# Kernel optimization log

Measured on AMD Instinct MI355X. Metric: run time of the kernel, lower is better.

## Reference

```python
import jax, jax.numpy as jnp
import numpy as np

SIZE = 84        # pupil size
SIZE_F = 167     # field grid size
X_PAD = 39       # pad for 90 -> 167
KNUM = 16        # number of phase kernels (== required batch size)
CENTER = 120     # center crop
NOISE = 0.003


def _disk_mask(M=SIZE, R=SIZE / 2.0):
    # get_amp: unit disk of radius R on an MxM grid
    x, y = np.meshgrid(np.arange(-(M - 1) / 2, M / 2), np.arange(-(M - 1) / 2, M / 2))
    return jnp.asarray((x ** 2 + y ** 2 <= R ** 2).astype(np.float32))


def setup_inputs() -> dict:
    key = jax.random.key(0)
    k1, k2, k3 = jax.random.split(key, 3)
    x = jax.random.uniform(k1, (16, 90, 90, 1), dtype=jnp.float32)
    P = jax.random.uniform(k2, (16, 84, 84), dtype=jnp.float32,
                           minval=-0.5 * np.pi, maxval=0.5 * np.pi)
    W3 = jax.random.normal(k3, (12800, 10), dtype=jnp.float32) * 0.01
    b3 = jnp.zeros((10,), dtype=jnp.float32)
    return {"x": x, "P": P, "W3": W3, "b3": b3}


def _forward(x, P, W3, b3):
    mask = _disk_mask()
    amp = jnp.sum(mask)  # normalization of the autocorrelation

    # --- input field: pad 90 -> 167, complex, fftshift/fft2/fftshift ---
    # NOTE: tf.signal.fftshift default shifts ALL axes (incl. batch); the two
    # shifts cancel on the batch axis, replicated faithfully here.
    xp = jnp.pad(x, ((0, 0), (X_PAD, X_PAD - 1), (X_PAD, X_PAD - 1), (0, 0)))[..., 0]
    xc = xp.astype(jnp.complex64)
    X = jnp.fft.fftshift(jnp.fft.fft2(jnp.fft.fftshift(xc)))  # [16,167,167]
    Xr = jnp.repeat(X, KNUM, axis=0)                          # [256,167,167]

    # --- OTF: FFT-accelerated autocorrelation of the pupil P_amp*exp(i*phase) ---
    Pc = (mask * jnp.cos(P) + 1j * mask * jnp.sin(P)).astype(jnp.complex64)  # [16,84,84]
    Pp = jnp.pad(Pc, ((0, 0), (42, 41), (42, 41)))                           # [16,167,167]
    F = jnp.fft.fft2(Pp)
    OTF = jnp.fft.fftshift(jnp.fft.ifft2(F * jnp.conj(F)))  # all-axes shift
    OTF = jnp.concatenate([OTF[8:], OTF[:8]], axis=0) / amp  # undoes batch roll

    # --- propagation: multiply in frequency domain, back to space ---
    y = Xr * jnp.tile(OTF, (KNUM, 1, 1))  # [256,167,167]
    y = jnp.fft.fftshift(jnp.fft.ifft2(jnp.fft.fftshift(y)))
    r = jnp.real(y).reshape(16, KNUM, SIZE_F, SIZE_F)
    # per image: kernels 0..7 minus kernels 8..15 -> channels
    d = jnp.transpose(r[:, :8] - r[:, 8:], (0, 2, 3, 1))  # [16,167,167,8]

    # additive noise (np.random in original; fixed key -> deterministic constant)
    d = d + NOISE * jax.random.normal(jax.random.key(42), d.shape, dtype=jnp.float32)

    # center crop, relu, 3x3/3 max-pool, flatten, softmax dense
    b = (SIZE_F + 1) // 2 - CENTER // 2  # 24
    c = jax.nn.relu(d[:, b:b + CENTER, b:b + CENTER, :])  # [16,120,120,8]
    pooled = jax.lax.reduce_window(c, -jnp.inf, jax.lax.max,
                                   (1, 3, 3, 1), (1, 3, 3, 1), 'VALID')  # [16,40,40,8]
    flat = pooled.reshape(16, -1)  # [16,12800]
    return jax.nn.softmax(flat @ W3 + b3)


def reference(x, P, W3, b3):
    return _forward(x, P, W3, b3)
```

## Files before the change

### kernel.cpp

```cpp
#include <hip/hip_runtime.h>
#include <math.h>

constexpr int N  = 167;
constexpr int NN = 167 * 167;
constexpr int NP = 90;
constexpr int MP = 84;
constexpr int CROP = 120;
constexpr int HCOL = 84;
constexpr int HALF_SZ = 1784896;

constexpr size_t SZ_MAT   = (size_t)NN * 2;
constexpr size_t OFF_M1   = 0;
constexpr size_t OFF_M1T  = OFF_M1 + SZ_MAT;
constexpr size_t OFF_WF   = OFF_M1T + SZ_MAT;
constexpr size_t OFF_M2   = OFF_WF + SZ_MAT;
constexpr size_t OFF_M2T  = OFF_M2 + SZ_MAT;
constexpr size_t OFF_M3   = OFF_M2T + SZ_MAT;
constexpr size_t OFF_M3T84= OFF_M3 + (size_t)CROP * N * 2;
constexpr size_t OFF_PHI2 = OFF_M3T84 + (size_t)HCOL * CROP * 2;
constexpr size_t OFF_AMP  = OFF_PHI2 + (size_t)N * 2;
constexpr size_t OFF_X    = OFF_AMP + 4;
constexpr size_t OFF_T1   = OFF_X  + (size_t)16 * N * HCOL * 2;
constexpr size_t OFF_A    = OFF_T1 + (size_t)16 * N * NP * 2;
constexpr size_t OFF_T2   = OFF_A  + (size_t)16 * NN * 2;
constexpr size_t OFF_BD   = OFF_T2 + (size_t)16 * N * MP * 2;
constexpr size_t OFF_T3   = OFF_BD + (size_t)8 * NN;
constexpr size_t OFF_OTF  = OFF_T3 + (size_t)8 * N * HCOL * 2;
constexpr size_t OFF_FLAT = OFF_OTF+ (size_t)8 * N * HCOL * 2;
constexpr size_t OFF_PC   = OFF_FLAT + (size_t)16 * 12800;
constexpr size_t WS_FLOATS = OFF_PC + (size_t)16 * MP * MP * 2;

__device__ __forceinline__ unsigned rotl32(unsigned x, int r) {
    return (x << r) | (x >> (32 - r));
}

__device__ float noise_at(unsigned idx) {
    unsigned c0, c1; int lane;
    if (idx < (unsigned)HALF_SZ) { c0 = idx; c1 = idx + HALF_SZ; lane = 0; }
    else                         { c0 = idx - HALF_SZ; c1 = idx; lane = 1; }
    const unsigned ks0 = 0u, ks1 = 42u, ks2 = 0x1BD11BDAu ^ 42u;
    unsigned x0 = c0 + ks0, x1 = c1 + ks1;
#define TFR(r) { x0 += x1; x1 = rotl32(x1, r); x1 ^= x0; }
    TFR(13) TFR(15) TFR(26) TFR(6)   x0 += ks1; x1 += ks2 + 1u;
    TFR(17) TFR(29) TFR(16) TFR(24)  x0 += ks2; x1 += ks0 + 2u;
    TFR(13) TFR(15) TFR(26) TFR(6)   x0 += ks0; x1 += ks1 + 3u;
    TFR(17) TFR(29) TFR(16) TFR(24)  x0 += ks1; x1 += ks2 + 4u;
    TFR(13) TFR(15) TFR(26) TFR(6)   x0 += ks2; x1 += ks0 + 5u;
#undef TFR
    unsigned bits = lane ? x1 : x0;
    float u01 = __uint_as_float((bits >> 9) | 0x3F800000u) - 1.0f;
    const float lo = -0.99999994f;
    float f = fmaxf(lo, u01 * 2.0f + lo);
    float w = -log1pf(-f * f);
    float p;
    if (w < 5.0f) {
        w -= 2.5f;
        p = 2.81022636e-08f;
        p = fmaf(p, w, 3.43273939e-07f);
        p = fmaf(p, w, -3.5233877e-06f);
        p = fmaf(p, w, -4.39150654e-06f);
        p = fmaf(p, w, 0.00021858087f);
        p = fmaf(p, w, -0.00125372503f);
        p = fmaf(p, w, -0.00417768164f);
        p = fmaf(p, w, 0.246640727f);
        p = fmaf(p, w, 1.50140941f);
    } else {
        w = sqrtf(w) - 3.0f;
        p = -0.000200214257f;
        p = fmaf(p, w, 0.000100950558f);
        p = fmaf(p, w, 0.00134934322f);
        p = fmaf(p, w, -0.00367342844f);
        p = fmaf(p, w, 0.00573950773f);
        p = fmaf(p, w, -0.0076224613f);
        p = fmaf(p, w, 0.00943887047f);
        p = fmaf(p, w, 1.00167406f);
        p = fmaf(p, w, 2.83297682f);
    }
    return 1.41421356237f * p * f;
}

__global__ void k_prep(const float* __restrict__ P, float* ws) {
    int bx = blockIdx.x, t = threadIdx.x;
    if (bx < 109) {
        __shared__ float2 wtab[N];
        const float TPI = (float)(6.283185307179586476925286766559 / 167.0);
        for (int i = t; i < N; i += 256) {
            float s, c; sincosf(TPI * (float)i, &s, &c);
            wtab[i] = make_float2(c, s);
        }
        __syncthreads();
        int id = bx * 256 + t;
        if (id >= NN) return;
        int k = id / N, m = id % N;
        const float inv = 1.0f / 167.0f;
        int t1 = ((k + 84) * ((m + 83) % N)) % N;
        float2 w1 = wtab[t1];
        ws[OFF_M1 + 2 * id] = w1.x;  ws[OFF_M1 + 2 * id + 1] = -w1.y;
        ws[OFF_M1T + 2 * (m * N + k)] = w1.x;  ws[OFF_M1T + 2 * (m * N + k) + 1] = -w1.y;
        int tw = (k * m) % N;
        float2 ww = wtab[tw];
        ws[OFF_WF + 2 * id] = ww.x;  ws[OFF_WF + 2 * id + 1] = -ww.y;
        int t2 = ((k + 84) * m) % N;
        float2 w2 = wtab[t2];
        ws[OFF_M2 + 2 * id] = w2.x * inv;  ws[OFF_M2 + 2 * id + 1] = w2.y * inv;
        ws[OFF_M2T + 2 * (m * N + k)] = w2.x * inv;  ws[OFF_M2T + 2 * (m * N + k) + 1] = w2.y * inv;
        if (k < CROP) {
            int t3 = ((k + 108) * ((m + 83) % N)) % N;
            float2 w3 = wtab[t3];
            ws[OFF_M3 + 2 * (k * N + m)] = w3.x * inv;  ws[OFF_M3 + 2 * (k * N + m) + 1] = w3.y * inv;
            if (m < HCOL) {
                ws[OFF_M3T84 + 2 * (m * CROP + k)] = w3.x * inv;
                ws[OFF_M3T84 + 2 * (m * CROP + k) + 1] = w3.y * inv;
            }
        }
        if (id < N) {
            float2 wp = wtab[(2 * id) % N];
            ws[OFF_PHI2 + 2 * id] = wp.x;
            ws[OFF_PHI2 + 2 * id + 1] = wp.y;
        }
    } else if (bx < 550) {
        int id = (bx - 109) * 256 + t;
        if (id >= 16 * MP * MP) return;
        int rc = id % (MP * MP);
        int r = rc / MP, c = rc % MP;
        float y = r - 41.5f, x = c - 41.5f;
        float2 v = {0.f, 0.f};
        if (x * x + y * y <= 1764.0f) {
            float sp, cp; sincosf(P[id], &sp, &cp);
            v.x = cp; v.y = sp;
        }
        ((float2*)(ws + OFF_PC))[id] = v;
    } else {
        __shared__ int red[256];
        int cnt = 0;
        for (int i = t; i < MP * MP; i += 256) {
            int r = i / MP, c = i % MP;
            float y = r - 41.5f, x = c - 41.5f;
            if (x * x + y * y <= 1764.0f) cnt++;
        }
        red[t] = cnt; __syncthreads();
        for (int s = 128; s > 0; s >>= 1) { if (t < s) red[t] += red[t + s]; __syncthreads(); }
        if (t == 0) ws[OFF_AMP] = (float)red[0];
    }
}

__global__ __launch_bounds__(128) void k_rows(const float* __restrict__ x, float* ws) {
    int kr = blockIdx.x, bj = blockIdx.y, t = threadIdx.x;
    __shared__ float2 wbuf[NP];
    if (blockIdx.z == 0) {
        const float2* M1 = (const float2*)(ws + OFF_M1);
        if (t < NP) wbuf[t] = M1[kr * N + 39 + t];
        __syncthreads();
        if (t >= NP) return;
        float2 acc = {0.f, 0.f};
        for (int nr = 0; nr < NP; nr++) {
            float2 w = wbuf[nr];
            float xv = x[(bj * NP + nr) * NP + t];
            acc.x += w.x * xv; acc.y += w.y * xv;
        }
        ((float2*)(ws + OFF_T1))[(bj * N + kr) * NP + t] = acc;
    } else {
        const float2* WF = (const float2*)(ws + OFF_WF);
        if (t < MP) wbuf[t] = WF[kr * N + 42 + t];
        __syncthreads();
        if (t >= MP) return;
        const float2* PC = (const float2*)(ws + OFF_PC) + (size_t)bj * MP * MP;
        float2 acc = {0.f, 0.f};
        for (int nr = 0; nr < MP; nr++) {
            float2 w = wbuf[nr];
            float2 pc = PC[nr * MP + t];
            acc.x += w.x * pc.x - w.y * pc.y;
            acc.y += w.x * pc.y + w.y * pc.x;
        }
        ((float2*)(ws + OFF_T2))[(bj * N + kr) * MP + t] = acc;
    }
}

constexpr int RCH = 6;
__global__ __launch_bounds__(192) void k_cols(float* ws) {
    int bj = blockIdx.y, tid = threadIdx.x;
    __shared__ __align__(16) float2 sbuf[RCH * MP];
    if (blockIdx.x < 84) {
        int k0 = blockIdx.x * 2;
        const float2* T1 = (const float2*)(ws + OFF_T1);
        for (int idx = tid; idx < 2 * NP; idx += 192) {
            int r = idx / NP, m = idx % NP;
            if (k0 + r < N) sbuf[r * NP + m] = T1[((size_t)bj * N + k0 + r) * NP + m];
        }
        __syncthreads();
        int col = tid % HCOL, grp = tid / HCOL;
        if (grp >= 2) return;
        int kr = k0 + grp;
        if (kr >= N) return;
        const float2* M1T = (const float2*)(ws + OFF_M1T);
        float2 acc = {0.f, 0.f};
#pragma unroll 5
        for (int ncp = 0; ncp < 45; ncp++) {
            int nc = 2 * ncp;
            float4 u = *(const float4*)&sbuf[grp * NP + nc];
            float2 w0 = M1T[(39 + nc) * N + col];
            float2 w1 = M1T[(40 + nc) * N + col];
            acc.x += u.x * w0.x - u.y * w0.y;
            acc.y += u.x * w0.y + u.y * w0.x;
            acc.x += u.z * w1.x - u.w * w1.y;
            acc.y += u.z * w1.y + u.w * w1.x;
        }
        ((float2*)(ws + OFF_X))[((size_t)bj * N + kr) * HCOL + col] = acc;
    } else {
        int i0 = (blockIdx.x - 84) * RCH;
        const float2* T2 = (const float2*)(ws + OFF_T2);
        for (int idx = tid; idx < RCH * MP; idx += 192) {
            int q = idx / MP, nc = idx % MP, kr = i0 + q;
            if (kr < N) sbuf[idx] = T2[(bj * N + kr) * MP + nc];
        }
        __syncthreads();
        if (tid >= N) return;
        const float2* WF = (const float2*)(ws + OFF_WF);
        float2 acc[RCH];
#pragma unroll
        for (int q = 0; q < RCH; q++) acc[q] = make_float2(0.f, 0.f);
        for (int ncp = 0; ncp < 42; ncp++) {
            int nc = 2 * ncp;
            float2 w0 = WF[(42 + nc) * N + tid];
            float2 w1 = WF[(43 + nc) * N + tid];
#pragma unroll
            for (int q = 0; q < RCH; q++) {
                float4 u = *(const float4*)&sbuf[q * MP + nc];
                acc[q].x += u.x * w0.x - u.y * w0.y;
                acc[q].y += u.x * w0.y + u.y * w0.x;
                acc[q].x += u.z * w1.x - u.w * w1.y;
                acc[q].y += u.z * w1.y + u.w * w1.x;
            }
        }
        float2* A = (float2*)(ws + OFF_A);
#pragma unroll
        for (int q = 0; q < RCH; q++)
            if (i0 + q < N) A[((size_t)bj * N + i0 + q) * N + tid] = acc[q];
    }
}

__global__ __launch_bounds__(192) void k2c(float* ws) {
    int chunk = blockIdx.x, c = blockIdx.y, tid = threadIdx.x;
    int k0 = chunk * 2;
    __shared__ float bds[2][N];
    const float2* A = (const float2*)(ws + OFF_A);
    float inv_amp = 1.0f / ws[OFF_AMP];
    for (int idx = tid; idx < 2 * N; idx += 192) {
        int r = idx / N, m = idx % N;
        int k = k0 + r;
        if (k < N) {
            float2 a0 = A[((size_t)c * N + k) * N + m];
            float2 a1 = A[((size_t)(c + 8) * N + k) * N + m];
            bds[r][m] = (a0.x * a0.x + a0.y * a0.y - a1.x * a1.x - a1.y * a1.y) * inv_amp;
        }
    }
    __syncthreads();
    int col = tid % HCOL, grp = tid / HCOL;
    if (grp >= 2) return;
    int k = k0 + grp;
    if (k >= N) return;
    const float2* M2T = (const float2*)(ws + OFF_M2T);
    float2 acc = {0.f, 0.f};
    for (int m = 0; m < N; m++) {
        float bv = bds[grp][m];
        float2 w = M2T[m * N + col];
        acc.x += w.x * bv; acc.y += w.y * bv;
    }
    ((float2*)(ws + OFF_T3))[((size_t)c * N + k) * HCOL + col] = acc;
}

__global__ __launch_bounds__(192) void k2d(float* ws) {
    int chunk = blockIdx.x, c = blockIdx.y, tid = threadIdx.x;
    int i0 = chunk * 2;
    __shared__ float2 m2s[2][N];
    const float2* M2 = (const float2*)(ws + OFF_M2);
    for (int idx = tid; idx < 2 * N; idx += 192) {
        int r = idx / N, k = idx % N;
        if (i0 + r < N) m2s[r][k] = M2[(i0 + r) * N + k];
    }
    __syncthreads();
    int col = tid % HCOL, grp = tid / HCOL;
    if (grp >= 2) return;
    int i = i0 + grp;
    if (i >= N) return;
    const float2* T3 = (const float2*)(ws + OFF_T3) + (size_t)c * N * HCOL;
    float2 acc = {0.f, 0.f};
    for (int k = 0; k < N; k++) {
        float2 w = m2s[grp][k];
        float2 u = T3[k * HCOL + col];
        acc.x += u.x * w.x - u.y * w.y;
        acc.y += u.x * w.y + u.y * w.x;
    }
    ((float2*)(ws + OFF_OTF))[((size_t)c * N + i) * HCOL + col] = acc;
}

constexpr int K34R = 12;
constexpr int KCH  = 12;
constexpr int NT34 = (N + KCH - 1) / KCH;

constexpr int SM_ZS   = 0;
constexpr int SM_M3C  = SM_ZS + 2 * KCH * HCOL * 2;
constexpr int SM_PHIS = SM_M3C + 2 * KCH * K34R * 2;
constexpr int SM_PM   = SM_PHIS + N * 2;
constexpr int SM_TOT  = SM_PM + 4 * CROP;

constexpr int ZBUF = KCH * HCOL;
constexpr int MBUF = KCH * K34R;

#define K34_FMA_BODY(kl)                                                        \
    {                                                                           \
        float4 zz = *(const float4*)&zcur[(kl) * HCOL + 2 * pair];              \
        float4 wa = *(const float4*)&mcur[(kl) * K34R + r0];                    \
        a00.x += wa.x * zz.x - wa.y * zz.y;  a00.y += wa.x * zz.y + wa.y * zz.x;\
        a01.x += wa.x * zz.z - wa.y * zz.w;  a01.y += wa.x * zz.w + wa.y * zz.z;\
        a10.x += wa.z * zz.x - wa.w * zz.y;  a10.y += wa.z * zz.y + wa.w * zz.x;\
        a11.x += wa.z * zz.z - wa.w * zz.w;  a11.y += wa.z * zz.w + wa.w * zz.z;\
    }

__global__ __launch_bounds__(256) void k34(float* ws) {
    int chunk = blockIdx.x, c = blockIdx.y, b = blockIdx.z, tid = threadIdx.x;
    int i0 = chunk * K34R;
    __shared__ __align__(16) float smem[SM_TOT];
    float2* zbase = (float2*)(smem + SM_ZS);
    float2* mbase = (float2*)(smem + SM_M3C);
    float2* phis  = (float2*)(smem + SM_PHIS);
    float*  pmf   = smem + SM_PM;
    float2 (*us)[HCOL] = (float2 (*)[HCOL])(smem + SM_ZS);

    const float2* M3 = (const float2*)(ws + OFF_M3);
    const float4* X4   = (const float4*)(ws + OFF_X   + (size_t)b * N * HCOL * 2);
    const float4* OTF4 = (const float4*)(ws + OFF_OTF + (size_t)c * N * HCOL * 2);
    for (int idx = tid; idx < N; idx += 256) phis[idx] = ((const float2*)(ws + OFF_PHI2))[idx];

    int qkl[2], qcp[2];
#pragma unroll
    for (int e = 0; e < 2; e++) {
        int idx = tid + e * 256;
        qkl[e] = idx / 42; qcp[e] = idx - qkl[e] * 42;
    }
    int mkl = tid % 12, mr = tid / 12;

    int pair = tid % 42, grp = tid / 42;
    int r0 = grp * 2;
    float2 a00 = {0.f,0.f}, a01 = {0.f,0.f}, a10 = {0.f,0.f}, a11 = {0.f,0.f};

    float4 xq[2], oq[2];
    float2 m3r;

#pragma unroll
    for (int e = 0; e < 2; e++)
        if (qkl[e] < KCH) { xq[e] = X4[qkl[e] * 42 + qcp[e]]; oq[e] = OTF4[qkl[e] * 42 + qcp[e]]; }
    if (tid < 144) m3r = M3[(i0 + mr) * N + mkl];
#pragma unroll
    for (int e = 0; e < 2; e++)
        if (qkl[e] < KCH) {
            float4 z;
            z.x = xq[e].x * oq[e].x - xq[e].y * oq[e].y;
            z.y = xq[e].x * oq[e].y + xq[e].y * oq[e].x;
            z.z = xq[e].z * oq[e].z - xq[e].w * oq[e].w;
            z.w = xq[e].z * oq[e].w + xq[e].w * oq[e].z;
            *(float4*)&zbase[qkl[e] * HCOL + 2 * qcp[e]] = z;
        }
    if (tid < 144) mbase[mkl * K34R + mr] = m3r;
    __syncthreads();

    for (int t = 0; t < NT34; t++) {
        int cbuf = t & 1, nbuf = cbuf ^ 1;
        int kr0 = t * KCH;
        int chn = min(KCH, N - kr0);
        int nbase = kr0 + KCH;
        int nchn = (t + 1 < NT34) ? (N - nbase < KCH ? N - nbase : KCH) : 0;
        if (nchn > 0) {
#pragma unroll
            for (int e = 0; e < 2; e++)
                if (qkl[e] < nchn) { xq[e] = X4[(nbase + qkl[e]) * 42 + qcp[e]];
                                     oq[e] = OTF4[(nbase + qkl[e]) * 42 + qcp[e]]; }
            if (tid < 144 && mkl < nchn) m3r = M3[(i0 + mr) * N + nbase + mkl];
        }
        const float2* zcur = zbase + cbuf * ZBUF;
        const float2* mcur = mbase + cbuf * MBUF;
        if (grp < 6) {
            if (chn == KCH) {
#pragma unroll
                for (int kl = 0; kl < KCH; kl++) K34_FMA_BODY(kl)
            } else {
#pragma unroll
                for (int kl = 0; kl < KCH - 1; kl++) K34_FMA_BODY(kl)
            }
        }
        if (nchn > 0) {
            float2* znxt = zbase + nbuf * ZBUF;
            float2* mnxt = mbase + nbuf * MBUF;
#pragma unroll
            for (int e = 0; e < 2; e++)
                if (qkl[e] < nchn) {
                    float4 z;
                    z.x = xq[e].x * oq[e].x - xq[e].y * oq[e].y;
                    z.y = xq[e].x * oq[e].y + xq[e].y * oq[e].x;
                    z.z = xq[e].z * oq[e].z - xq[e].w * oq[e].w;
                    z.w = xq[e].z * oq[e].w + xq[e].w * oq[e].z;
                    *(float4*)&znxt[qkl[e] * HCOL + 2 * qcp[e]] = z;
                }
            if (tid < 144 && mkl < nchn) mnxt[mkl * K34R + mr] = m3r;
        }
        __syncthreads();
    }

    if (grp < 6) {
        *(float4*)&us[r0][2 * pair]     = make_float4(a00.x, a00.y, a01.x, a01.y);
        *(float4*)&us[r0 + 1][2 * pair] = make_float4(a10.x, a10.y, a11.x, a11.y);
    }
    __syncthreads();

    if (tid < 240) {
        int grp2 = tid / CROP, j = tid % CROP;
        int rbase = grp2 * 6;
        const float2* M3T84 = (const float2*)(ws + OFF_M3T84);
        float2 A[6]; float Bq[6];
#pragma unroll
        for (int q = 0; q < 6; q++) A[q] = make_float2(0.f, 0.f);
#pragma unroll 4
        for (int ncp = 0; ncp < 41; ncp++) {
            int nc = 2 * ncp;
            float2 w0 = M3T84[nc * CROP + j];
            float2 w1 = M3T84[(nc + 1) * CROP + j];
#pragma unroll
            for (int q = 0; q < 6; q++) {
                float4 u = *(const float4*)&us[rbase + q][nc];
                A[q].x += u.x * w0.x - u.y * w0.y;
                A[q].y += u.x * w0.y + u.y * w0.x;
                A[q].x += u.z * w1.x - u.w * w1.y;
                A[q].y += u.z * w1.y + u.w * w1.x;
            }
        }
        {
            float2 w = M3T84[82 * CROP + j];
#pragma unroll
            for (int q = 0; q < 6; q++) {
                float2 u = us[rbase + q][82];
                A[q].x += u.x * w.x - u.y * w.y;
                A[q].y += u.x * w.y + u.y * w.x;
            }
        }
        {
            float2 w = M3T84[(HCOL - 1) * CROP + j];
#pragma unroll
            for (int q = 0; q < 6; q++) {
                float2 u = us[rbase + q][HCOL - 1];
                Bq[q] = u.x * w.x - u.y * w.y;
            }
        }
#pragma unroll
        for (int g = 0; g < 2; g++) {
            float vmax = 0.f;
#pragma unroll
            for (int r = 0; r < 3; r++) {
                int q = g * 3 + r, i = i0 + rbase + q;
                int s = i + j + 49; if (s >= N) s -= N;
                float2 ph = phis[s];
                float val = A[q].x * (1.0f + ph.x) - A[q].y * ph.y + Bq[q];
                unsigned idx = (((unsigned)b * N + (24 + i)) * N + (24 + j)) * 8u + c;
                val += 0.003f * noise_at(idx);
                vmax = fmaxf(vmax, val);
            }
            pmf[(grp2 * 2 + g) * CROP + j] = vmax;
        }
    }
    __syncthreads();
    if (tid < 160) {
        int pr = tid / 40, pc = tid % 40;
        float m = fmaxf(fmaxf(pmf[pr * CROP + 3 * pc], pmf[pr * CROP + 3 * pc + 1]),
                        pmf[pr * CROP + 3 * pc + 2]);
        int prow = chunk * 4 + pr;
        ws[OFF_FLAT + (size_t)b * 12800 + ((size_t)prow * 40 + pc) * 8 + c] = m;
    }
}

__global__ void k5(const float* __restrict__ W3, const float* __restrict__ b3,
                   const float* __restrict__ ws, float* __restrict__ out) {
    int b = blockIdx.x, t = threadIdx.x;
    __shared__ float red[256][10];
    float acc[10];
#pragma unroll
    for (int o = 0; o < 10; o++) acc[o] = 0.f;
    const float* fl = ws + OFF_FLAT + (size_t)b * 12800;
    for (int f = t; f < 12800; f += 256) {
        float v = fl[f];
#pragma unroll
        for (int o = 0; o < 10; o++) acc[o] = fmaf(v, W3[f * 10 + o], acc[o]);
    }
#pragma unroll
    for (int o = 0; o < 10; o++) red[t][o] = acc[o];
    __syncthreads();
    for (int s = 128; s > 0; s >>= 1) {
        if (t < s) {
#pragma unroll
            for (int o = 0; o < 10; o++) red[t][o] += red[t + s][o];
        }
        __syncthreads();
    }
    if (t == 0) {
        float lg[10], mx = -1e30f;
#pragma unroll
        for (int o = 0; o < 10; o++) { lg[o] = red[0][o] + b3[o]; mx = fmaxf(mx, lg[o]); }
        float sum = 0.f;
#pragma unroll
        for (int o = 0; o < 10; o++) { lg[o] = expf(lg[o] - mx); sum += lg[o]; }
#pragma unroll
        for (int o = 0; o < 10; o++) out[b * 10 + o] = lg[o] / sum;
    }
}

extern "C" void kernel_launch(void* const* d_in, const int* in_sizes, int n_in,
                              void* d_out, int out_size, void* d_ws, size_t ws_size,
                              hipStream_t stream) {
    const float* x  = (const float*)d_in[0];
    const float* P  = (const float*)d_in[1];
    const float* W3 = (const float*)d_in[2];
    const float* b3 = (const float*)d_in[3];
    float* ws  = (float*)d_ws;
    float* out = (float*)d_out;

    k_prep<<<551, 256, 0, stream>>>(P, ws);
    k_rows<<<dim3(N, 16, 2), 128, 0, stream>>>(x, ws);
    k_cols<<<dim3(84 + 28, 16), 192, 0, stream>>>(ws);
    k2c<<<dim3(84, 8), 192, 0, stream>>>(ws);
    k2d<<<dim3(84, 8), 192, 0, stream>>>(ws);
    k34<<<dim3(CROP / K34R, 8, 16), 256, 0, stream>>>(ws);
    k5<<<16, 256, 0, stream>>>(W3, b3, ws, out);
}
```

Baseline: 205.7 us.

## Fuse row/column DFT stages and OTF squaring into fewer kernels

Merges the separate row and column DFT passes for the input field into one kernel that keeps the intermediate in shared memory. It also fuses the pupil DFT, the squared-magnitude difference and the first inverse OTF pass into a single kernel, which drops the A buffer round trip and two launches. Twiddle-table prep now writes the transposed matrices with coalesced indexing in separate blocks, and M2 is read from M2T. The cost is less parallelism per launch, and the pupil rows are recomputed per block pair.

```diff
diff --git a/kernel.cpp b/kernel.cpp
--- a/kernel.cpp
+++ b/kernel.cpp
@@ -81,7 +81,7 @@
 
 __global__ void k_prep(const float* __restrict__ P, float* ws) {
     int bx = blockIdx.x, t = threadIdx.x;
-    if (bx < 109) {
+    if (bx < 258) {
         __shared__ float2 wtab[N];
         const float TPI = (float)(6.283185307179586476925286766559 / 167.0);
         for (int i = t; i < N; i += 256) {
@@ -89,37 +89,49 @@
             wtab[i] = make_float2(c, s);
         }
         __syncthreads();
-        int id = bx * 256 + t;
-        if (id >= NN) return;
-        int k = id / N, m = id % N;
         const float inv = 1.0f / 167.0f;
-        int t1 = ((k + 84) * ((m + 83) % N)) % N;
-        float2 w1 = wtab[t1];
-        ws[OFF_M1 + 2 * id] = w1.x;  ws[OFF_M1 + 2 * id + 1] = -w1.y;
-        ws[OFF_M1T + 2 * (m * N + k)] = w1.x;  ws[OFF_M1T + 2 * (m * N + k) + 1] = -w1.y;
-        int tw = (k * m) % N;
-        float2 ww = wtab[tw];
-        ws[OFF_WF + 2 * id] = ww.x;  ws[OFF_WF + 2 * id + 1] = -ww.y;
-        int t2 = ((k + 84) * m) % N;
-        float2 w2 = wtab[t2];
-        ws[OFF_M2 + 2 * id] = w2.x * inv;  ws[OFF_M2 + 2 * id + 1] = w2.y * inv;
-        ws[OFF_M2T + 2 * (m * N + k)] = w2.x * inv;  ws[OFF_M2T + 2 * (m * N + k) + 1] = w2.y * inv;
-        if (k < CROP) {
-            int t3 = ((k + 108) * ((m + 83) % N)) % N;
+        if (bx < 109) {
+            int id = bx * 256 + t;
+            if (id >= NN) return;
+            int k = id / N, m = id % N;
+            int t1 = ((k + 84) * ((m + 83) % N)) % N;
+            float2 w1 = wtab[t1];
+            ws[OFF_M1 + 2 * id] = w1.x;  ws[OFF_M1 + 2 * id + 1] = -w1.y;
+            int tw = (k * m) % N;
+            float2 ww = wtab[tw];
+            ws[OFF_WF + 2 * id] = ww.x;  ws[OFF_WF + 2 * id + 1] = -ww.y;
+            if (k < CROP) {
+                int t3 = ((k + 108) * ((m + 83) % N)) % N;
+                float2 w3 = wtab[t3];
+                ws[OFF_M3 + 2 * (k * N + m)] = w3.x * inv;
+                ws[OFF_M3 + 2 * (k * N + m) + 1] = w3.y * inv;
+            }
+            if (id < N) {
+                float2 wp = wtab[(2 * id) % N];
+                ws[OFF_PHI2 + 2 * id] = wp.x;
+                ws[OFF_PHI2 + 2 * id + 1] = wp.y;
+            }
+        } else if (bx < 218) {
+            int id = (bx - 109) * 256 + t;
+            if (id >= NN) return;
+            int m = id / N, k = id % N;
+            int t1 = ((k + 84) * ((m + 83) % N)) % N;
+            float2 w1 = wtab[t1];
+            ws[OFF_M1T + 2 * id] = w1.x;  ws[OFF_M1T + 2 * id + 1] = -w1.y;
+            int t2 = ((k + 84) * m) % N;
+            float2 w2 = wtab[t2];
+            ws[OFF_M2T + 2 * id] = w2.x * inv;  ws[OFF_M2T + 2 * id + 1] = w2.y * inv;
+        } else {
+            int id = (bx - 218) * 256 + t;
+            if (id >= HCOL * CROP) return;
+            int m = id / CROP, kk = id % CROP;
+            int t3 = ((kk + 108) * ((m + 83) % N)) % N;
             float2 w3 = wtab[t3];
-            ws[OFF_M3 + 2 * (k * N + m)] = w3.x * inv;  ws[OFF_M3 + 2 * (k * N + m) + 1] = w3.y * inv;
-            if (m < HCOL) {
-                ws[OFF_M3T84 + 2 * (m * CROP + k)] = w3.x * inv;
-                ws[OFF_M3T84 + 2 * (m * CROP + k) + 1] = w3.y * inv;
-            }
-        }
-        if (id < N) {
-            float2 wp = wtab[(2 * id) % N];
-            ws[OFF_PHI2 + 2 * id] = wp.x;
-            ws[OFF_PHI2 + 2 * id + 1] = wp.y;
-        }
-    } else if (bx < 550) {
-        int id = (bx - 109) * 256 + t;
+            ws[OFF_M3T84 + 2 * id] = w3.x * inv;
+            ws[OFF_M3T84 + 2 * id + 1] = w3.y * inv;
+        }
+    } else if (bx < 699) {
+        int id = (bx - 258) * 256 + t;
         if (id >= 16 * MP * MP) return;
         int rc = id % (MP * MP);
         int r = rc / MP, c = rc % MP;
@@ -144,139 +156,128 @@
     }
 }
 
-__global__ __launch_bounds__(128) void k_rows(const float* __restrict__ x, float* ws) {
-    int kr = blockIdx.x, bj = blockIdx.y, t = threadIdx.x;
-    __shared__ float2 wbuf[NP];
-    if (blockIdx.z == 0) {
-        const float2* M1 = (const float2*)(ws + OFF_M1);
-        if (t < NP) wbuf[t] = M1[kr * N + 39 + t];
-        __syncthreads();
-        if (t >= NP) return;
-        float2 acc = {0.f, 0.f};
-        for (int nr = 0; nr < NP; nr++) {
-            float2 w = wbuf[nr];
-            float xv = x[(bj * NP + nr) * NP + t];
-            acc.x += w.x * xv; acc.y += w.y * xv;
-        }
-        ((float2*)(ws + OFF_T1))[(bj * N + kr) * NP + t] = acc;
-    } else {
-        const float2* WF = (const float2*)(ws + OFF_WF);
-        if (t < MP) wbuf[t] = WF[kr * N + 42 + t];
-        __syncthreads();
-        if (t >= MP) return;
-        const float2* PC = (const float2*)(ws + OFF_PC) + (size_t)bj * MP * MP;
-        float2 acc = {0.f, 0.f};
-        for (int nr = 0; nr < MP; nr++) {
-            float2 w = wbuf[nr];
-            float2 pc = PC[nr * MP + t];
-            acc.x += w.x * pc.x - w.y * pc.y;
-            acc.y += w.x * pc.y + w.y * pc.x;
-        }
-        ((float2*)(ws + OFF_T2))[(bj * N + kr) * MP + t] = acc;
-    }
-}
-
-constexpr int RCH = 6;
-__global__ __launch_bounds__(192) void k_cols(float* ws) {
-    int bj = blockIdx.y, tid = threadIdx.x;
-    __shared__ __align__(16) float2 sbuf[RCH * MP];
-    if (blockIdx.x < 84) {
-        int k0 = blockIdx.x * 2;
-        const float2* T1 = (const float2*)(ws + OFF_T1);
-        for (int idx = tid; idx < 2 * NP; idx += 192) {
-            int r = idx / NP, m = idx % NP;
-            if (k0 + r < N) sbuf[r * NP + m] = T1[((size_t)bj * N + k0 + r) * NP + m];
-        }
-        __syncthreads();
-        int col = tid % HCOL, grp = tid / HCOL;
-        if (grp >= 2) return;
-        int kr = k0 + grp;
-        if (kr >= N) return;
-        const float2* M1T = (const float2*)(ws + OFF_M1T);
-        float2 acc = {0.f, 0.f};
-#pragma unroll 5
-        for (int ncp = 0; ncp < 45; ncp++) {
-            int nc = 2 * ncp;
-            float4 u = *(const float4*)&sbuf[grp * NP + nc];
-            float2 w0 = M1T[(39 + nc) * N + col];
-            float2 w1 = M1T[(40 + nc) * N + col];
-            acc.x += u.x * w0.x - u.y * w0.y;
-            acc.y += u.x * w0.y + u.y * w0.x;
-            acc.x += u.z * w1.x - u.w * w1.y;
-            acc.y += u.z * w1.y + u.w * w1.x;
-        }
-        ((float2*)(ws + OFF_X))[((size_t)bj * N + kr) * HCOL + col] = acc;
-    } else {
-        int i0 = (blockIdx.x - 84) * RCH;
-        const float2* T2 = (const float2*)(ws + OFF_T2);
-        for (int idx = tid; idx < RCH * MP; idx += 192) {
-            int q = idx / MP, nc = idx % MP, kr = i0 + q;
-            if (kr < N) sbuf[idx] = T2[(bj * N + kr) * MP + nc];
-        }
-        __syncthreads();
-        if (tid >= N) return;
-        const float2* WF = (const float2*)(ws + OFF_WF);
-        float2 acc[RCH];
-#pragma unroll
-        for (int q = 0; q < RCH; q++) acc[q] = make_float2(0.f, 0.f);
-        for (int ncp = 0; ncp < 42; ncp++) {
-            int nc = 2 * ncp;
-            float2 w0 = WF[(42 + nc) * N + tid];
-            float2 w1 = WF[(43 + nc) * N + tid];
-#pragma unroll
-            for (int q = 0; q < RCH; q++) {
-                float4 u = *(const float4*)&sbuf[q * MP + nc];
-                acc[q].x += u.x * w0.x - u.y * w0.y;
-                acc[q].y += u.x * w0.y + u.y * w0.x;
-                acc[q].x += u.z * w1.x - u.w * w1.y;
-                acc[q].y += u.z * w1.y + u.w * w1.x;
-            }
-        }
-        float2* A = (float2*)(ws + OFF_A);
-#pragma unroll
-        for (int q = 0; q < RCH; q++)
-            if (i0 + q < N) A[((size_t)bj * N + i0 + q) * N + tid] = acc[q];
-    }
-}
-
-__global__ __launch_bounds__(192) void k2c(float* ws) {
-    int chunk = blockIdx.x, c = blockIdx.y, tid = threadIdx.x;
-    int k0 = chunk * 2;
-    __shared__ float bds[2][N];
-    const float2* A = (const float2*)(ws + OFF_A);
-    float inv_amp = 1.0f / ws[OFF_AMP];
-    for (int idx = tid; idx < 2 * N; idx += 192) {
-        int r = idx / N, m = idx % N;
-        int k = k0 + r;
-        if (k < N) {
-            float2 a0 = A[((size_t)c * N + k) * N + m];
-            float2 a1 = A[((size_t)(c + 8) * N + k) * N + m];
-            bds[r][m] = (a0.x * a0.x + a0.y * a0.y - a1.x * a1.x - a1.y * a1.y) * inv_amp;
+__global__ __launch_bounds__(192) void k_rcx(const float* __restrict__ x, float* ws) {
+    int kp = blockIdx.x, bj = blockIdx.y, tid = threadIdx.x;
+    int k0 = kp * 2;
+    __shared__ float2 m1w[2][NP];
+    __shared__ __align__(16) float2 t1s[2][NP];
+    const float2* M1 = (const float2*)(ws + OFF_M1);
+    for (int idx = tid; idx < 2 * NP; idx += 192) {
+        int r = idx / NP, m = idx % NP;
+        if (k0 + r < N) m1w[r][m] = M1[(k0 + r) * N + 39 + m];
+    }
+    __syncthreads();
+    {
+        int grp = tid / 96, tcol = tid % 96;
+        if (tcol < NP && k0 + grp < N) {
+            float2 acc = {0.f, 0.f};
+            for (int nr = 0; nr < NP; nr++) {
+                float2 w = m1w[grp][nr];
+                float xv = x[(bj * NP + nr) * NP + tcol];
+                acc.x += w.x * xv; acc.y += w.y * xv;
+            }
+            t1s[grp][tcol] = acc;
         }
     }
     __syncthreads();
     int col = tid % HCOL, grp = tid / HCOL;
     if (grp >= 2) return;
-    int k = k0 + grp;
-    if (k >= N) return;
-    const float2* M2T = (const float2*)(ws + OFF_M2T);
+    int kr = k0 + grp;
+    if (kr >= N) return;
+    const float2* M1T = (const float2*)(ws + OFF_M1T);
     float2 acc = {0.f, 0.f};
-    for (int m = 0; m < N; m++) {
-        float bv = bds[grp][m];
-        float2 w = M2T[m * N + col];
-        acc.x += w.x * bv; acc.y += w.y * bv;
-    }
-    ((float2*)(ws + OFF_T3))[((size_t)c * N + k) * HCOL + col] = acc;
+#pragma unroll 5
+    for (int ncp = 0; ncp < 45; ncp++) {
+        int nc = 2 * ncp;
+        float4 u = *(const float4*)&t1s[grp][nc];
+        float2 w0 = M1T[(39 + nc) * N + col];
+        float2 w1 = M1T[(40 + nc) * N + col];
+        acc.x += u.x * w0.x - u.y * w0.y;
+        acc.y += u.x * w0.y + u.y * w0.x;
+        acc.x += u.z * w1.x - u.w * w1.y;
+        acc.y += u.z * w1.y + u.w * w1.x;
+    }
+    ((float2*)(ws + OFF_X))[((size_t)bj * N + kr) * HCOL + col] = acc;
+}
+
+__global__ __launch_bounds__(192) void k_rca(float* ws) {
+    int kp = blockIdx.x, c = blockIdx.y, tid = threadIdx.x;
+    int k0 = kp * 2;
+    __shared__ float2 wfw[2][MP];
+    __shared__ __align__(16) float2 t2s[2][2][MP];
+    __shared__ float bds[2][N];
+    const float2* WF = (const float2*)(ws + OFF_WF);
+    for (int idx = tid; idx < 2 * MP; idx += 192) {
+        int r = idx / MP, m = idx % MP;
+        if (k0 + r < N) wfw[r][m] = WF[(k0 + r) * N + 42 + m];
+    }
+    __syncthreads();
+#pragma unroll
+    for (int pass = 0; pass < 2; pass++) {
+        int jj = (pass == 0) ? c : c + 8;
+        int grp = tid / 96, tcol = tid % 96;
+        if (tcol < MP && k0 + grp < N) {
+            const float2* PC = (const float2*)(ws + OFF_PC) + (size_t)jj * MP * MP;
+            float2 acc = {0.f, 0.f};
+            for (int nr = 0; nr < MP; nr++) {
+                float2 w = wfw[grp][nr];
+                float2 pc = PC[nr * MP + tcol];
+                acc.x += w.x * pc.x - w.y * pc.y;
+                acc.y += w.x * pc.y + w.y * pc.x;
+            }
+            t2s[pass][grp][tcol] = acc;
+        }
+    }
+    __syncthreads();
+    if (tid < N) {
+        float inv_amp = 1.0f / ws[OFF_AMP];
+#pragma unroll
+        for (int rr = 0; rr < 2; rr++) {
+            if (k0 + rr < N) {
+                float2 a0 = {0.f, 0.f}, a1 = {0.f, 0.f};
+                for (int ncp = 0; ncp < 42; ncp++) {
+                    int nc = 2 * ncp;
+                    float2 w0 = WF[(42 + nc) * N + tid];
+                    float2 w1 = WF[(43 + nc) * N + tid];
+                    float4 u0 = *(const float4*)&t2s[0][rr][nc];
+                    a0.x += u0.x * w0.x - u0.y * w0.y;
+                    a0.y += u0.x * w0.y + u0.y * w0.x;
+                    a0.x += u0.z * w1.x - u0.w * w1.y;
+                    a0.y += u0.z * w1.y + u0.w * w1.x;
+                    float4 u1 = *(const float4*)&t2s[1][rr][nc];
+                    a1.x += u1.x * w0.x - u1.y * w0.y;
+                    a1.y += u1.x * w0.y + u1.y * w0.x;
+                    a1.x += u1.z * w1.x - u1.w * w1.y;
+                    a1.y += u1.z * w1.y + u1.w * w1.x;
+                }
+                bds[rr][tid] = (a0.x * a0.x + a0.y * a0.y - a1.x * a1.x - a1.y * a1.y) * inv_amp;
+            }
+        }
+    }
+    __syncthreads();
+    {
+        int grp = tid / 96, col = tid % 96;
+        if (col < HCOL && k0 + grp < N) {
+            const float2* M2T = (const float2*)(ws + OFF_M2T);
+            float2 acc = {0.f, 0.f};
+            for (int m = 0; m < N; m++) {
+                float bv = bds[grp][m];
+                float2 w = M2T[m * N + col];
+                acc.x += w.x * bv; acc.y += w.y * bv;
+            }
+            ((float2*)(ws + OFF_T3))[((size_t)c * N + k0 + grp) * HCOL + col] = acc;
+        }
+    }
 }
 
 __global__ __launch_bounds__(192) void k2d(float* ws) {
     int chunk = blockIdx.x, c = blockIdx.y, tid = threadIdx.x;
     int i0 = chunk * 2;
     __shared__ float2 m2s[2][N];
-    const float2* M2 = (const float2*)(ws + OFF_M2);
+    const float2* M2T = (const float2*)(ws + OFF_M2T);
     for (int idx = tid; idx < 2 * N; idx += 192) {
         int r = idx / N, k = idx % N;
-        if (i0 + r < N) m2s[r][k] = M2[(i0 + r) * N + k];
+        if (i0 + r < N) m2s[r][k] = M2T[k * N + (i0 + r)];
     }
     __syncthreads();
     int col = tid % HCOL, grp = tid / HCOL;
@@ -521,10 +522,9 @@
     float* ws  = (float*)d_ws;
     float* out = (float*)d_out;
 
-    k_prep<<<551, 256, 0, stream>>>(P, ws);
-    k_rows<<<dim3(N, 16, 2), 128, 0, stream>>>(x, ws);
-    k_cols<<<dim3(84 + 28, 16), 192, 0, stream>>>(ws);
-    k2c<<<dim3(84, 8), 192, 0, stream>>>(ws);
+    k_prep<<<700, 256, 0, stream>>>(P, ws);
+    k_rcx<<<dim3(84, 16), 192, 0, stream>>>(x, ws);
+    k_rca<<<dim3(84, 8), 192, 0, stream>>>(ws);
     k2d<<<dim3(84, 8), 192, 0, stream>>>(ws);
     k34<<<dim3(CROP / K34R, 8, 16), 256, 0, stream>>>(ws);
     k5<<<16, 256, 0, stream>>>(W3, b3, ws, out);
```

Result: faster. 199.5 us (-3.0%).
